# Kernel optimization log

Hardware: AMD Instinct MI355X
Metric: run time of the kernel (lower is better)

Reference implementation:

```python
import jax, jax.numpy as jnp
import numpy as np

D = 1024  # input_dim == output_dim
B = 4096  # batch (acts as sequence for batch-wise self-attention)


def setup_inputs() -> dict:
    key = jax.random.key(0)
    k1, k2, k3, k4 = jax.random.split(key, 4)
    inputs = jax.random.normal(k1, (B, D), dtype=jnp.float32)
    rotation_params = jax.random.normal(k2, (D, D), dtype=jnp.float32)
    # torch nn.Linear(input_dim, output_dim): weight (out, in), bias (out,)
    linear_w = jax.random.normal(k3, (D, D), dtype=jnp.float32) * (1.0 / np.sqrt(D))
    linear_b = jax.random.normal(k4, (D,), dtype=jnp.float32) * 0.01
    return {"inputs": inputs, "rotation_params": rotation_params,
            "linear_w": linear_w, "linear_b": linear_b}


def reference(inputs, rotation_params, linear_w, linear_b):
    # query = X R ; key = X R^T  -> scores = softmax(Q K^T / sqrt(D)) over batch dim
    query = inputs @ rotation_params                 # [B, D]
    key = inputs @ rotation_params.T                 # [B, D]
    scale = 1.0 / np.sqrt(D).astype(np.float32)
    scores = jax.nn.softmax(jnp.einsum('bd,cd->bc', query, key) * scale, axis=-1)  # [B, B]
    weighted = scores @ inputs                        # [B, D]
    return weighted @ linear_w.T + linear_b           # [B, out]
```

## Files before the change

### kernel.cpp

```cpp
#include <hip/hip_runtime.h>
#include <math.h>
#include <stdint.h>

using f16 = _Float16;
using half8 = __attribute__((ext_vector_type(8))) f16;
using half4 = __attribute__((ext_vector_type(4))) f16;
using f32x4 = __attribute__((ext_vector_type(4))) float;

__device__ __forceinline__ void gl_lds16(const f16* g, f16* l) {
  __builtin_amdgcn_global_load_lds(
      (const __attribute__((address_space(1))) void*)g,
      (__attribute__((address_space(3))) void*)l, 16, 0, 0);
}

__global__ __launch_bounds__(512, 2) void gemm_q2(
    const f16* __restrict__ Ap, const f16* __restrict__ Bp,
    f16* __restrict__ Ch, long sCp, int N, int K, long sAp, long sBp,
    float scale) {
  __shared__ f16 lds[2 * 4096 * 8];
  const int tid = threadIdx.x;
  const int lane = tid & 63;
  const int wave = tid >> 6;
  const int wr = (wave >> 2) * 128;
  const int wc = (wave & 3) * 64;

  const int nwg = gridDim.x * gridDim.y;
  int bid = blockIdx.y * gridDim.x + blockIdx.x;
  bid = (bid & 7) * (nwg >> 3) + (bid >> 3);
  const int bm = (bid / gridDim.x) * 256;
  const int bn = (bid % gridDim.x) * 256;

  const int nt = K / 32;

  auto stage = [&](int t, int i) {
    const int g0 = i * 512 + wave * 64;
    const int ga = g0 + lane;
    const bool isB = ga >= 2048;
    const int gl = ga & 2047;
    const int pl = gl >> 10;
    const int gp = gl & 1023;
    const int r = gp >> 2;
    const int cg = (gp & 3) ^ ((r >> 1) & 3);
    const f16* gs = (isB ? Bp + (size_t)pl * sBp + (size_t)(bn + r) * K
                         : Ap + (size_t)pl * sAp + (size_t)(bm + r) * K) +
                    t * 32 + cg * 8;
    gl_lds16(gs, &lds[((size_t)(t & 1) * 4096 + g0) * 8]);
  };

  int aoff[2][8], boff[2][4];
#pragma unroll
  for (int pl = 0; pl < 2; ++pl) {
#pragma unroll
    for (int fr = 0; fr < 8; ++fr) {
      const int row = wr + fr * 16 + (lane & 15);
      const int kg = (lane >> 4) ^ ((row >> 1) & 3);
      aoff[pl][fr] = (pl * 1024 + row * 4 + kg) * 8;
    }
#pragma unroll
    for (int fc = 0; fc < 4; ++fc) {
      const int col = wc + fc * 16 + (lane & 15);
      const int kg = (lane >> 4) ^ ((col >> 1) & 3);
      boff[pl][fc] = (2048 + pl * 1024 + col * 4 + kg) * 8;
    }
  }

  f32x4 acc[8][4];
#pragma unroll
  for (int m = 0; m < 8; ++m)
#pragma unroll
    for (int n = 0; n < 4; ++n) acc[m][n] = (f32x4){0.f, 0.f, 0.f, 0.f};

  half8 af0[2][4], af1[2][4], bf0[2][2], bf1[2][2];

#define LOAD_A(dst, h)                                          \
  _Pragma("unroll") for (int pl = 0; pl < 2; ++pl)              \
      _Pragma("unroll") for (int i = 0; i < 4; ++i) dst[pl][i] = \
          *(const half8*)&buf[aoff[pl][(h) * 4 + i]];
#define LOAD_B(dst, h)                                          \
  _Pragma("unroll") for (int pl = 0; pl < 2; ++pl)              \
      _Pragma("unroll") for (int j = 0; j < 2; ++j) dst[pl][j] = \
          *(const half8*)&buf[boff[pl][(h) * 2 + j]];
#define MFMA_Q(A, B, ah, bh)                                                  \
  _Pragma("unroll") for (int i = 0; i < 4; ++i)                               \
      _Pragma("unroll") for (int j = 0; j < 2; ++j) {                         \
    f32x4& c = acc[(ah) * 4 + i][(bh) * 2 + j];                               \
    c = __builtin_amdgcn_mfma_f32_16x16x32_f16(A[0][i], B[0][j], c, 0, 0, 0); \
    c = __builtin_amdgcn_mfma_f32_16x16x32_f16(A[0][i], B[1][j], c, 0, 0, 0); \
    c = __builtin_amdgcn_mfma_f32_16x16x32_f16(A[1][i], B[0][j], c, 0, 0, 0); \
  }
#define SBAR0() __builtin_amdgcn_sched_barrier(0)

#pragma unroll
  for (int i = 0; i < 8; ++i) stage(0, i);

  for (int t = 0; t < nt; ++t) {
    const f16* buf = &lds[(size_t)(t & 1) * 4096 * 8];
    asm volatile("s_waitcnt vmcnt(0)" ::: "memory");
    asm volatile("s_barrier" ::: "memory");
    const bool pf = (t + 1 < nt);

    LOAD_A(af0, 0);
    LOAD_B(bf0, 0);
    if (pf) { stage(t + 1, 0); stage(t + 1, 1); stage(t + 1, 2); stage(t + 1, 3); }
    SBAR0();
    LOAD_B(bf1, 1);
    SBAR0();
    __builtin_amdgcn_s_setprio(1);
    MFMA_Q(af0, bf0, 0, 0);
    __builtin_amdgcn_s_setprio(0);
    SBAR0();
    LOAD_A(af1, 1);
    if (pf) { stage(t + 1, 4); stage(t + 1, 5); stage(t + 1, 6); stage(t + 1, 7); }
    SBAR0();
    __builtin_amdgcn_s_setprio(1);
    MFMA_Q(af0, bf1, 0, 1);
    __builtin_amdgcn_s_setprio(0);
    SBAR0();
    LOAD_B(bf0, 0);
    SBAR0();
    __builtin_amdgcn_s_setprio(1);
    MFMA_Q(af1, bf1, 1, 1);
    __builtin_amdgcn_s_setprio(0);
    SBAR0();
    __builtin_amdgcn_s_setprio(1);
    MFMA_Q(af1, bf0, 1, 0);
    __builtin_amdgcn_s_setprio(0);
    SBAR0();
  }
#undef LOAD_A
#undef LOAD_B
#undef MFMA_Q
#undef SBAR0

#pragma unroll
  for (int m = 0; m < 8; ++m) {
#pragma unroll
    for (int n = 0; n < 4; ++n) {
      const int col = bn + wc + n * 16 + (lane & 15);
#pragma unroll
      for (int q = 0; q < 4; ++q) {
        const int row = bm + wr + m * 16 + (lane >> 4) * 4 + q;
        const float v = acc[m][n][q] * scale;
        const f16 h = (f16)v;
        Ch[(size_t)row * N + col] = h;
        Ch[sCp + (size_t)row * N + col] = (f16)(v - (float)h);
      }
    }
  }
}

template <int NP, int EPI, bool BIASF>
__global__ __launch_bounds__(512, 2) void gemm_dp(
    const f16* __restrict__ Ap, const f16* __restrict__ Bp,
    void* __restrict__ Cv, const float* __restrict__ bias, int M, int N, int K,
    long sAp, long sBp, long sCp, float scale) {
  __shared__ f16 lds[3 * 2048 * 8];
  const int tid = threadIdx.x;
  const int lane = tid & 63;
  const int wave = tid >> 6;
  const int wr = (wave >> 1) * 32;
  const int wc = (wave & 1) * 64;

  const int nwg = gridDim.x * gridDim.y;
  int bid = blockIdx.y * gridDim.x + blockIdx.x;
  bid = (bid & 7) * (nwg >> 3) + (bid >> 3);
  const int bm = (bid / gridDim.x) * 128;
  const int bn = (bid % gridDim.x) * 128;

  constexpr int KSTEP = (NP == 2) ? 32 : 64;
  const int nt = K / KSTEP;

  auto stage = [&](int t, int i) {
    const int g0 = i * 512 + wave * 64;
    const int ga = g0 + lane;
    const bool isB = ga >= 1024;
    const int gl = ga & 1023;
    const int pl = gl >> 9;
    const int gp = gl & 511;
    const int r = gp >> 2;
    const int cg = (gp & 3) ^ ((r >> 1) & 3);
    const long sP = (NP == 2) ? (isB ? sBp : sAp) : 0;
    const int kOff = (NP == 2) ? 0 : pl * 32;
    const f16* gs = (isB ? Bp : Ap) + (size_t)pl * sP +
                    (size_t)((isB ? bn : bm) + r) * K + t * KSTEP + kOff +
                    cg * 8;
    gl_lds16(gs, &lds[((size_t)(t % 3) * 2048 + g0) * 8]);
  };

  int aoff[2][2], boff[2][4];
#pragma unroll
  for (int pl = 0; pl < 2; ++pl) {
#pragma unroll
    for (int m = 0; m < 2; ++m) {
      const int row = wr + m * 16 + (lane & 15);
      const int kg = (lane >> 4) ^ ((row >> 1) & 3);
      aoff[pl][m] = (pl * 512 + row * 4 + kg) * 8;
    }
#pragma unroll
    for (int n = 0; n < 4; ++n) {
      const int col = wc + n * 16 + (lane & 15);
      const int kg = (lane >> 4) ^ ((col >> 1) & 3);
      boff[pl][n] = (1024 + pl * 512 + col * 4 + kg) * 8;
    }
  }

  f32x4 acc[2][4];
#pragma unroll
  for (int m = 0; m < 2; ++m)
#pragma unroll
    for (int n = 0; n < 4; ++n) acc[m][n] = (f32x4){0.f, 0.f, 0.f, 0.f};

#pragma unroll
  for (int i = 0; i < 4; ++i) stage(0, i);
#pragma unroll
  for (int i = 0; i < 4; ++i) stage(1, i);

  for (int t = 0; t < nt; ++t) {
    const f16* buf = &lds[(size_t)(t % 3) * 2048 * 8];
    if (t + 1 < nt)
      asm volatile("s_waitcnt vmcnt(4)" ::: "memory");
    else
      asm volatile("s_waitcnt vmcnt(0)" ::: "memory");
    asm volatile("s_barrier" ::: "memory");

    half8 af[2][2], bf[2][4];
#pragma unroll
    for (int pl = 0; pl < 2; ++pl) {
#pragma unroll
      for (int m = 0; m < 2; ++m) af[pl][m] = *(const half8*)&buf[aoff[pl][m]];
#pragma unroll
      for (int n = 0; n < 4; ++n) bf[pl][n] = *(const half8*)&buf[boff[pl][n]];
    }
    if (t + 2 < nt) {
      stage(t + 2, 0);
      stage(t + 2, 1);
      stage(t + 2, 2);
      stage(t + 2, 3);
    }
    __builtin_amdgcn_sched_barrier(0);
    __builtin_amdgcn_s_setprio(1);
#pragma unroll
    for (int m = 0; m < 2; ++m) {
#pragma unroll
      for (int n = 0; n < 4; ++n) {
        acc[m][n] = __builtin_amdgcn_mfma_f32_16x16x32_f16(af[0][m], bf[0][n],
                                                           acc[m][n], 0, 0, 0);
        if (NP == 2) {
          acc[m][n] = __builtin_amdgcn_mfma_f32_16x16x32_f16(
              af[0][m], bf[1][n], acc[m][n], 0, 0, 0);
          acc[m][n] = __builtin_amdgcn_mfma_f32_16x16x32_f16(
              af[1][m], bf[0][n], acc[m][n], 0, 0, 0);
        } else {
          acc[m][n] = __builtin_amdgcn_mfma_f32_16x16x32_f16(
              af[1][m], bf[1][n], acc[m][n], 0, 0, 0);
        }
      }
    }
    __builtin_amdgcn_s_setprio(0);
    __builtin_amdgcn_sched_barrier(0);
  }

#pragma unroll
  for (int m = 0; m < 2; ++m) {
#pragma unroll
    for (int n = 0; n < 4; ++n) {
      const int col = bn + wc + n * 16 + (lane & 15);
      const float bv = BIASF ? bias[col] : 0.f;
#pragma unroll
      for (int q = 0; q < 4; ++q) {
        const int row = bm + wr + m * 16 + (lane >> 4) * 4 + q;
        float v = acc[m][n][q] * scale;
        if (EPI == 0) {
          ((float*)Cv)[(size_t)row * N + col] = v + bv;
        } else if (EPI == 1) {
          f16* C = (f16*)Cv;
          const f16 h = (f16)v;
          C[(size_t)row * N + col] = h;
          C[sCp + (size_t)row * N + col] = (f16)(v - (float)h);
        } else {
          ((f16*)Cv)[(size_t)row * N + col] = (f16)v;
        }
      }
    }
  }
}

template <int NP, int TN, int EPI, bool BIASF, int MINW>
__global__ __launch_bounds__(256, MINW) void gemm_mp(
    const f16* __restrict__ Ap, const f16* __restrict__ Bp,
    void* __restrict__ Cv, const float* __restrict__ bias, int M, int N, int K,
    long sAp, long sBp, long sCp, float scale) {
  constexpr int FR = (TN == 128) ? 4 : 2;
  constexpr int FC = 4;
  constexpr int AG = NP * 512;
  constexpr int BPG = TN * 4;
  __shared__ f16 As[NP * 128 * 32];
  __shared__ f16 Bs[NP * TN * 32];
  const int tid = threadIdx.x;
  const int lane = tid & 63;
  const int wave = tid >> 6;
  const int wr = (TN == 128) ? (wave >> 1) * 64 : wave * 32;
  const int wc = (TN == 128) ? (wave & 1) * 64 : 0;

  const int nwg = gridDim.x * gridDim.y;
  int bid = blockIdx.y * gridDim.x + blockIdx.x;
  bid = (bid & 7) * (nwg >> 3) + (bid >> 3);
  const int bm = (bid / gridDim.x) * 128;
  const int bn = (bid % gridDim.x) * TN;

  int aoff[NP][FR], boff[NP][FC];
#pragma unroll
  for (int p = 0; p < NP; ++p) {
#pragma unroll
    for (int m = 0; m < FR; ++m) {
      const int row = wr + m * 16 + (lane & 15);
      const int kga = (lane >> 4) ^ ((row >> 1) & 3);
      aoff[p][m] = (p * 512 + row * 4 + kga) * 8;
    }
#pragma unroll
    for (int n = 0; n < FC; ++n) {
      const int col = wc + n * 16 + (lane & 15);
      const int kgb = (lane >> 4) ^ ((col >> 1) & 3);
      boff[p][n] = (p * BPG + col * 4 + kgb) * 8;
    }
  }

  f32x4 acc[FR][FC];
#pragma unroll
  for (int m = 0; m < FR; ++m)
#pragma unroll
    for (int n = 0; n < FC; ++n) acc[m][n] = (f32x4){0.f, 0.f, 0.f, 0.f};

  for (int k0 = 0; k0 < K; k0 += 32) {
#pragma unroll
    for (int i = 0; i < (NP * (512 + TN * 4)) / 256; ++i) {
      const int g0 = i * 256 + wave * 64;
      const bool isB = g0 >= AG;
      const int ga0 = g0 - (isB ? AG : 0);
      const int ga = ga0 + lane;
      const int pl = isB ? (ga / BPG) : (ga >> 9);
      const int gp = isB ? (ga % BPG) : (ga & 511);
      const int r = gp >> 2;
      const int cg = (gp & 3) ^ ((r >> 1) & 3);
      const f16* gs = (isB ? Bp + (size_t)pl * sBp + (size_t)(bn + r) * K
                           : Ap + (size_t)pl * sAp + (size_t)(bm + r) * K) +
                      k0 + cg * 8;
      f16* ld = (isB ? Bs : As) + (size_t)ga0 * 8;
      gl_lds16(gs, ld);
    }
    __syncthreads();

    half8 af[NP][FR], bf[NP][FC];
#pragma unroll
    for (int p = 0; p < NP; ++p) {
#pragma unroll
      for (int m = 0; m < FR; ++m) af[p][m] = *(const half8*)&As[aoff[p][m]];
#pragma unroll
      for (int n = 0; n < FC; ++n) bf[p][n] = *(const half8*)&Bs[boff[p][n]];
    }
#pragma unroll
    for (int m = 0; m < FR; ++m) {
#pragma unroll
      for (int n = 0; n < FC; ++n) {
        acc[m][n] = __builtin_amdgcn_mfma_f32_16x16x32_f16(af[0][m], bf[0][n],
                                                           acc[m][n], 0, 0, 0);
        if (NP == 2) {
          acc[m][n] = __builtin_amdgcn_mfma_f32_16x16x32_f16(
              af[0][m], bf[1][n], acc[m][n], 0, 0, 0);
          acc[m][n] = __builtin_amdgcn_mfma_f32_16x16x32_f16(
              af[1][m], bf[0][n], acc[m][n], 0, 0, 0);
        }
      }
    }
    __syncthreads();
  }

#pragma unroll
  for (int m = 0; m < FR; ++m) {
#pragma unroll
    for (int n = 0; n < FC; ++n) {
      const int col = bn + wc + n * 16 + (lane & 15);
      const float bv = BIASF ? bias[col] : 0.f;
#pragma unroll
      for (int q = 0; q < 4; ++q) {
        const int row = bm + wr + m * 16 + (lane >> 4) * 4 + q;
        float v = acc[m][n][q] * scale;
        if (EPI == 0) {
          ((float*)Cv)[(size_t)row * N + col] = v + bv;
        } else if (EPI == 1) {
          f16* C = (f16*)Cv;
          const f16 h = (f16)v;
          C[(size_t)row * N + col] = h;
          C[sCp + (size_t)row * N + col] = (f16)(v - (float)h);
        } else {
          ((f16*)Cv)[(size_t)row * N + col] = (f16)v;
        }
      }
    }
  }
}

__global__ __launch_bounds__(256) void split_fused(
    const float* __restrict__ X, const float* __restrict__ R,
    const float* __restrict__ W, f16* __restrict__ Xp, f16* __restrict__ Rp,
    f16* __restrict__ Wp, long sX, long sR) {
  const int b = blockIdx.x;
  const float* in;
  f16* out;
  long ps;
  int np, i;
  if (b < 4096) {
    in = X; out = Xp; ps = sX; np = 2; i = b * 256 + threadIdx.x;
  } else if (b < 5120) {
    in = R; out = Rp; ps = sR; np = 2; i = (b - 4096) * 256 + threadIdx.x;
  } else {
    in = W; out = Wp; ps = 0; np = 1; i = (b - 5120) * 256 + threadIdx.x;
  }
  const float4 v = ((const float4*)in)[i];
  const float vv[4] = {v.x, v.y, v.z, v.w};
  half4 h, mm;
#pragma unroll
  for (int q = 0; q < 4; ++q) {
    h[q] = (f16)vv[q];
    mm[q] = (f16)(vv[q] - (float)h[q]);
  }
  ((half4*)out)[i] = h;
  if (np == 2) ((half4*)(out + ps))[i] = mm;
}

__global__ __launch_bounds__(256) void split_t2(const float* __restrict__ in,
                                                f16* __restrict__ out, int Mr,
                                                int Nc, long planeStride) {
  __shared__ float Ls[64][65];
  const int i0 = blockIdx.y * 64;
  const int j0 = blockIdx.x * 64;
  const int t = threadIdx.x;
  const int r = t >> 4;
  const int c = (t & 15) * 4;
#pragma unroll
  for (int i = 0; i < 4; ++i) {
    const float4 v =
        *(const float4*)&in[(size_t)(i0 + r + i * 16) * Nc + j0 + c];
    Ls[r + i * 16][c + 0] = v.x;
    Ls[r + i * 16][c + 1] = v.y;
    Ls[r + i * 16][c + 2] = v.z;
    Ls[r + i * 16][c + 3] = v.w;
  }
  __syncthreads();
#pragma unroll
  for (int i = 0; i < 4; ++i) {
    const int r2 = r + i * 16;
    half4 h, mm;
#pragma unroll
    for (int q = 0; q < 4; ++q) {
      const float v = Ls[c + q][r2];
      h[q] = (f16)v;
      mm[q] = (f16)(v - (float)h[q]);
    }
    *(half4*)&out[(size_t)(j0 + r2) * Mr + i0 + c] = h;
    *(half4*)&out[planeStride + (size_t)(j0 + r2) * Mr + i0 + c] = mm;
  }
}

__global__ __launch_bounds__(256) void softmax_ps(const f16* __restrict__ Lh,
                                                  long sL,
                                                  f16* __restrict__ P) {
  __shared__ float row[4096];
  __shared__ float red[8];
  const int rix = blockIdx.x;
  const f16* ph = Lh + (size_t)rix * 4096;
  const f16* pm = ph + sL;
  f16* o = P + (size_t)rix * 4096;
  const int tid = threadIdx.x;

  float mx = -INFINITY;
  for (int i = tid * 8; i < 4096; i += 2048) {
    const half8 h = *(const half8*)&ph[i];
    const half8 mseg = *(const half8*)&pm[i];
#pragma unroll
    for (int q = 0; q < 8; ++q) {
      const float v = (float)h[q] + (float)mseg[q];
      row[i + q] = v;
      mx = fmaxf(mx, v);
    }
  }
#pragma unroll
  for (int off = 32; off > 0; off >>= 1) mx = fmaxf(mx, __shfl_xor(mx, off));
  if ((tid & 63) == 0) red[tid >> 6] = mx;
  __syncthreads();
  mx = fmaxf(fmaxf(red[0], red[1]), fmaxf(red[2], red[3]));

  float s = 0.f;
  for (int i = tid * 4; i < 4096; i += 1024) {
    float4 v = *reinterpret_cast<const float4*>(&row[i]);
    v.x = expf(v.x - mx);
    v.y = expf(v.y - mx);
    v.z = expf(v.z - mx);
    v.w = expf(v.w - mx);
    s += v.x + v.y + v.z + v.w;
    *reinterpret_cast<float4*>(&row[i]) = v;
  }
#pragma unroll
  for (int off = 32; off > 0; off >>= 1) s += __shfl_xor(s, off);
  if ((tid & 63) == 0) red[4 + (tid >> 6)] = s;
  __syncthreads();
  s = red[4] + red[5] + red[6] + red[7];
  const float inv = 1.0f / s;

  for (int i = tid * 8; i < 4096; i += 2048) {
    half8 h;
#pragma unroll
    for (int q = 0; q < 8; ++q) h[q] = (f16)(row[i + q] * inv);
    *(half8*)&o[i] = h;
  }
}

extern "C" void kernel_launch(void* const* d_in, const int* in_sizes, int n_in,
                              void* d_out, int out_size, void* d_ws,
                              size_t ws_size, hipStream_t stream) {
  const float* X = (const float*)d_in[0];
  const float* R = (const float*)d_in[1];
  const float* Wl = (const float*)d_in[2];
  const float* bias = (const float*)d_in[3];
  float* out = (float*)d_out;

  const int Bq = 4096, D = 1024;
  const size_t MiB = 1 << 20;
  uint8_t* w8 = (uint8_t*)d_ws;
  f16* Xp = (f16*)(w8);
  f16* Tp = (f16*)(w8 + 16 * MiB);
  f16* Yt = (f16*)(w8 + 32 * MiB);
  f16* Wp = (f16*)(w8 + 40 * MiB);
  f16* Rp = (f16*)(w8 + 42 * MiB);
  f16* Rtp = (f16*)(w8 + 46 * MiB);
  f16* Mtp = (f16*)(w8 + 50 * MiB);
  f16* Lh = (f16*)(w8 + 54 * MiB);
  f16* Pp = (f16*)(w8);

  const long sR = (long)D * D, sX = (long)Bq * D;
  const long sL = (long)Bq * Bq;
  const dim3 blk(256), blk512(512);

  split_fused<<<dim3(6144), blk, 0, stream>>>(X, R, Wl, Xp, Rp, Wp, sX, sR);
  split_t2<<<dim3(D / 64, D / 64), blk, 0, stream>>>(R, Rtp, D, D, sR);

  gemm_mp<2, 64, 1, false, 2><<<dim3(D / 64, D / 128), blk, 0, stream>>>(
      Rtp, Rp, Mtp, nullptr, D, D, D, sR, sR, sR, 1.f);
  gemm_dp<1, 2, false><<<dim3(Bq / 128, D / 128), blk512, 0, stream>>>(
      Wp, Xp, Yt, nullptr, D, Bq, D, 0, 0, 0, 1.f);
  gemm_dp<2, 1, false><<<dim3(D / 128, Bq / 128), blk512, 0, stream>>>(
      Xp, Mtp, Tp, nullptr, Bq, D, D, sX, sR, sX, 1.f);
  gemm_q2<<<dim3(Bq / 256, Bq / 256), blk512, 0, stream>>>(
      Tp, Xp, Lh, sL, Bq, D, sX, sX, 0.03125f);
  softmax_ps<<<dim3(Bq), blk, 0, stream>>>(Lh, sL, Pp);
  gemm_dp<1, 0, true><<<dim3(D / 128, Bq / 128), blk512, 0, stream>>>(
      Pp, Yt, out, bias, Bq, D, Bq, 0, 0, 0, 1.f);
}
```

Before: 226.0 us.

## Switch split-fp16 score GEMM to 32x32x16 MFMA with k-major LDS layout

New measurement: 259.5 us. +14.8%, slower.

```diff
diff --git a/kernel.cpp b/kernel.cpp
--- a/kernel.cpp
+++ b/kernel.cpp
@@ -6,6 +6,7 @@
 using half8 = __attribute__((ext_vector_type(8))) f16;
 using half4 = __attribute__((ext_vector_type(4))) f16;
 using f32x4 = __attribute__((ext_vector_type(4))) float;
+using f32x16 = __attribute__((ext_vector_type(16))) float;
 
 __device__ __forceinline__ void gl_lds16(const f16* g, f16* l) {
   __builtin_amdgcn_global_load_lds(
@@ -39,54 +40,66 @@
     const int gl = ga & 2047;
     const int pl = gl >> 10;
     const int gp = gl & 1023;
-    const int r = gp >> 2;
-    const int cg = (gp & 3) ^ ((r >> 1) & 3);
+    const int kgc = gp >> 8;
+    const int r = gp & 255;
     const f16* gs = (isB ? Bp + (size_t)pl * sBp + (size_t)(bn + r) * K
                          : Ap + (size_t)pl * sAp + (size_t)(bm + r) * K) +
-                    t * 32 + cg * 8;
+                    t * 32 + kgc * 8;
     gl_lds16(gs, &lds[((size_t)(t & 1) * 4096 + g0) * 8]);
   };
 
-  int aoff[2][8], boff[2][4];
+  int aoff[2][4][2], boff[2][2][2];
 #pragma unroll
   for (int pl = 0; pl < 2; ++pl) {
 #pragma unroll
-    for (int fr = 0; fr < 8; ++fr) {
-      const int row = wr + fr * 16 + (lane & 15);
-      const int kg = (lane >> 4) ^ ((row >> 1) & 3);
-      aoff[pl][fr] = (pl * 1024 + row * 4 + kg) * 8;
-    }
-#pragma unroll
-    for (int fc = 0; fc < 4; ++fc) {
-      const int col = wc + fc * 16 + (lane & 15);
-      const int kg = (lane >> 4) ^ ((col >> 1) & 3);
-      boff[pl][fc] = (2048 + pl * 1024 + col * 4 + kg) * 8;
-    }
-  }
-
-  f32x4 acc[8][4];
-#pragma unroll
-  for (int m = 0; m < 8; ++m)
-#pragma unroll
-    for (int n = 0; n < 4; ++n) acc[m][n] = (f32x4){0.f, 0.f, 0.f, 0.f};
-
-  half8 af0[2][4], af1[2][4], bf0[2][2], bf1[2][2];
-
-#define LOAD_A(dst, h)                                          \
-  _Pragma("unroll") for (int pl = 0; pl < 2; ++pl)              \
-      _Pragma("unroll") for (int i = 0; i < 4; ++i) dst[pl][i] = \
-          *(const half8*)&buf[aoff[pl][(h) * 4 + i]];
-#define LOAD_B(dst, h)                                          \
-  _Pragma("unroll") for (int pl = 0; pl < 2; ++pl)              \
-      _Pragma("unroll") for (int j = 0; j < 2; ++j) dst[pl][j] = \
-          *(const half8*)&buf[boff[pl][(h) * 2 + j]];
-#define MFMA_Q(A, B, ah, bh)                                                  \
-  _Pragma("unroll") for (int i = 0; i < 4; ++i)                               \
-      _Pragma("unroll") for (int j = 0; j < 2; ++j) {                         \
-    f32x4& c = acc[(ah) * 4 + i][(bh) * 2 + j];                               \
-    c = __builtin_amdgcn_mfma_f32_16x16x32_f16(A[0][i], B[0][j], c, 0, 0, 0); \
-    c = __builtin_amdgcn_mfma_f32_16x16x32_f16(A[0][i], B[1][j], c, 0, 0, 0); \
-    c = __builtin_amdgcn_mfma_f32_16x16x32_f16(A[1][i], B[0][j], c, 0, 0, 0); \
+    for (int rt = 0; rt < 4; ++rt) {
+#pragma unroll
+      for (int kf = 0; kf < 2; ++kf) {
+        const int row = wr + rt * 32 + (lane & 31);
+        const int kgc = kf * 2 + (lane >> 5);
+        aoff[pl][rt][kf] = (pl * 1024 + kgc * 256 + row) * 8;
+      }
+    }
+#pragma unroll
+    for (int ct = 0; ct < 2; ++ct) {
+#pragma unroll
+      for (int kf = 0; kf < 2; ++kf) {
+        const int col = wc + ct * 32 + (lane & 31);
+        const int kgc = kf * 2 + (lane >> 5);
+        boff[pl][ct][kf] = (2048 + pl * 1024 + kgc * 256 + col) * 8;
+      }
+    }
+  }
+
+  f32x16 acc[4][2];
+#pragma unroll
+  for (int rt = 0; rt < 4; ++rt)
+#pragma unroll
+    for (int ct = 0; ct < 2; ++ct)
+#pragma unroll
+      for (int q = 0; q < 16; ++q) acc[rt][ct][q] = 0.f;
+
+  half8 a01[2][2][2], a23[2][2][2], b0[2][2], b1[2][2];
+
+#define LOAD_A(dst, rb)                                          \
+  _Pragma("unroll") for (int pl = 0; pl < 2; ++pl)               \
+      _Pragma("unroll") for (int r2 = 0; r2 < 2; ++r2)           \
+          _Pragma("unroll") for (int kf = 0; kf < 2; ++kf)       \
+              dst[pl][r2][kf] = *(const half8*)&buf[aoff[pl][(rb) + r2][kf]];
+#define LOAD_B(dst, ct)                                          \
+  _Pragma("unroll") for (int pl = 0; pl < 2; ++pl)               \
+      _Pragma("unroll") for (int kf = 0; kf < 2; ++kf)           \
+          dst[pl][kf] = *(const half8*)&buf[boff[pl][(ct)][kf]];
+#define MFMA_Q(A, B, rb, ct)                                                   \
+  _Pragma("unroll") for (int r2 = 0; r2 < 2; ++r2)                             \
+      _Pragma("unroll") for (int kf = 0; kf < 2; ++kf) {                       \
+    f32x16& c = acc[(rb) + r2][ct];                                            \
+    c = __builtin_amdgcn_mfma_f32_32x32x16_f16(A[0][r2][kf], B[0][kf], c, 0,   \
+                                               0, 0);                          \
+    c = __builtin_amdgcn_mfma_f32_32x32x16_f16(A[0][r2][kf], B[1][kf], c, 0,   \
+                                               0, 0);                          \
+    c = __builtin_amdgcn_mfma_f32_32x32x16_f16(A[1][r2][kf], B[0][kf], c, 0,   \
+                                               0, 0);                          \
   }
 #define SBAR0() __builtin_amdgcn_sched_barrier(0)
 
@@ -99,31 +112,31 @@
     asm volatile("s_barrier" ::: "memory");
     const bool pf = (t + 1 < nt);
 
-    LOAD_A(af0, 0);
-    LOAD_B(bf0, 0);
+    LOAD_A(a01, 0);
+    LOAD_B(b0, 0);
     if (pf) { stage(t + 1, 0); stage(t + 1, 1); stage(t + 1, 2); stage(t + 1, 3); }
     SBAR0();
-    LOAD_B(bf1, 1);
+    LOAD_B(b1, 1);
     SBAR0();
     __builtin_amdgcn_s_setprio(1);
-    MFMA_Q(af0, bf0, 0, 0);
+    MFMA_Q(a01, b0, 0, 0);
     __builtin_amdgcn_s_setprio(0);
     SBAR0();
-    LOAD_A(af1, 1);
+    LOAD_A(a23, 2);
     if (pf) { stage(t + 1, 4); stage(t + 1, 5); stage(t + 1, 6); stage(t + 1, 7); }
     SBAR0();
     __builtin_amdgcn_s_setprio(1);
-    MFMA_Q(af0, bf1, 0, 1);
+    MFMA_Q(a01, b1, 0, 1);
     __builtin_amdgcn_s_setprio(0);
     SBAR0();
-    LOAD_B(bf0, 0);
+    LOAD_B(b0, 0);
     SBAR0();
     __builtin_amdgcn_s_setprio(1);
-    MFMA_Q(af1, bf1, 1, 1);
+    MFMA_Q(a23, b1, 2, 1);
     __builtin_amdgcn_s_setprio(0);
     SBAR0();
     __builtin_amdgcn_s_setprio(1);
-    MFMA_Q(af1, bf0, 1, 0);
+    MFMA_Q(a23, b0, 2, 0);
     __builtin_amdgcn_s_setprio(0);
     SBAR0();
   }
@@ -133,14 +146,15 @@
 #undef SBAR0
 
 #pragma unroll
-  for (int m = 0; m < 8; ++m) {
-#pragma unroll
-    for (int n = 0; n < 4; ++n) {
-      const int col = bn + wc + n * 16 + (lane & 15);
-#pragma unroll
-      for (int q = 0; q < 4; ++q) {
-        const int row = bm + wr + m * 16 + (lane >> 4) * 4 + q;
-        const float v = acc[m][n][q] * scale;
+  for (int rt = 0; rt < 4; ++rt) {
+#pragma unroll
+    for (int ct = 0; ct < 2; ++ct) {
+      const int col = bn + wc + ct * 32 + (lane & 31);
+#pragma unroll
+      for (int reg = 0; reg < 16; ++reg) {
+        const int row = bm + wr + rt * 32 + (reg & 3) + 8 * (reg >> 2) +
+                        4 * (lane >> 5);
+        const float v = acc[rt][ct][reg] * scale;
         const f16 h = (f16)v;
         Ch[(size_t)row * N + col] = h;
         Ch[sCp + (size_t)row * N + col] = (f16)(v - (float)h);
```
